# Optimization experiments

Hardware: AMD Instinct MI355X
Metric: run time of the kernel (lower is better)

Reference implementation:

```python
import jax, jax.numpy as jnp
import numpy as np
import math

NSEG = 4
SAMPLE_RATE = 16  # curve samples per bezier segment
SHARPNESS = 150.0


def _control_radians():
    n = NSEG
    theta = math.pi * 2 / (4 * n) + math.atan(math.tan(2 * math.pi / (4 * n)) / 3)
    r = []
    for i in range(n):
        r += [2 * math.pi / n * i, 2 * math.pi / n * i + theta, 2 * math.pi / n * (i + 1) - theta]
    return jnp.asarray(np.asarray(r, dtype=np.float32).reshape(n, 3))


def sdf_extruded_bezier(quaternion, translation, points, control_polygon, bez_weights, height):
    # quaternion [B,K,4], translation [B,K,3], points [B,M,3],
    # control_polygon [B,K,nseg,3,2], bez_weights [B,K,nseg,2], height [B,K]
    B, K, _ = quaternion.shape
    p = points[:, :, None, :] - translation[:, None, :, :]            # [B,M,K,3]
    q = quaternion[:, None, :, :]
    qn = q / jnp.sqrt(jnp.sum(q * q, -1, keepdims=True) + 1e-8)
    w, qv = qn[..., :1], -qn[..., 1:]                                  # conjugate -> world->local
    t2 = 2.0 * jnp.cross(qv, p)
    pl = p + w * t2 + jnp.cross(qv, t2)                                # local coords [B,M,K,3]
    p2d, pz = pl[..., :2], pl[..., 2]
    # rational cubic bezier per segment: P0,P1,P2 from this segment, P3 = next segment's P0
    P0 = control_polygon[:, :, :, 0, :]
    P1 = control_polygon[:, :, :, 1, :]
    P2 = control_polygon[:, :, :, 2, :]
    P3 = jnp.roll(P0, -1, axis=2)
    ts = jnp.linspace(0.0, 1.0, SAMPLE_RATE, endpoint=False)           # [S]
    b0 = (1 - ts) ** 3
    b1 = 3 * (1 - ts) ** 2 * ts
    b2 = 3 * (1 - ts) * ts ** 2
    b3 = ts ** 3
    w1 = bez_weights[..., 0:1]                                          # [B,K,nseg,1]
    w2 = bez_weights[..., 1:2]
    den = b0 + w1 * b1 + w2 * b2 + b3                                   # [B,K,nseg,S]
    num = (P0[..., None, :] * b0[:, None]
           + P1[..., None, :] * (w1[..., None] * b1[:, None])
           + P2[..., None, :] * (w2[..., None] * b2[:, None])
           + P3[..., None, :] * b3[:, None])                            # [B,K,nseg,S,2]
    curve = (num / den[..., None]).reshape(B, K, NSEG * SAMPLE_RATE, 2)
    rel = curve[:, None] - p2d[..., None, :]                            # [B,M,K,S*nseg,2]
    d2 = jnp.sum(rel * rel, -1)
    dmin = jnp.sqrt(jnp.min(d2, -1) + 1e-12)                            # unsigned 2D distance
    nxt = jnp.roll(rel, -1, axis=-2)
    cross = rel[..., 0] * nxt[..., 1] - rel[..., 1] * nxt[..., 0]
    dot = jnp.sum(rel * nxt, -1)
    winding = jnp.sum(jnp.arctan2(cross, dot), -1) / (2 * math.pi)
    sdf2d = jnp.where(jnp.abs(winding) > 0.5, -dmin, dmin)
    dz = jnp.abs(pz) - jnp.abs(height)[:, None, :]
    sdf = (jnp.minimum(jnp.maximum(sdf2d, dz), 0.0)
           + jnp.sqrt(jnp.maximum(sdf2d, 0.0) ** 2 + jnp.maximum(dz, 0.0) ** 2 + 1e-12))
    return sdf, dmin


def setup_inputs() -> dict:
    key = jax.random.key(0)
    k1, k2, k3, k4 = jax.random.split(key, 4)
    B, M, K, C = 4, 2048, 64, 64
    P = 4 + 3 + 1 + NSEG * 3 + NSEG * 2  # 28
    return {
        "sample_point_coordinates": jax.random.uniform(k1, (B, M, 3), jnp.float32, -1.0, 1.0),
        "primitive_parameters": 0.3 * jax.random.normal(k2, (B, P, K), jnp.float32),
        "intersection_layer_weights": jax.random.uniform(k3, (B, K, C), jnp.float32),
        "union_layer_weights": jax.random.uniform(k4, (B, C), jnp.float32),
        "is_training": 1,
    }


def reference(sample_point_coordinates, primitive_parameters, intersection_layer_weights, union_layer_weights, is_training):
    pp = jnp.swapaxes(primitive_parameters, 1, 2)                       # [B,K,P]
    B, K, _ = pp.shape
    quaternion = pp[..., :4]
    translation = pp[..., 4:7]
    height = pp[..., 7]
    radius = jnp.abs(pp[..., 8:8 + NSEG * 3]).reshape(B, K, NSEG, 3)
    rad = _control_radians()[None, None]                                # [1,1,nseg,3]
    control_polygon = jnp.stack([jnp.cos(rad) * radius, jnp.sin(rad) * radius], -1)
    bez_weights = jnp.abs(pp[..., 8 + NSEG * 3:]).reshape(B, K, NSEG, 2)
    primitive_sdf, support_distances = sdf_extruded_bezier(
        quaternion, translation, sample_point_coordinates, control_polygon, bez_weights, height)
    primitive_occ = jax.nn.sigmoid(-primitive_sdf * SHARPNESS)          # [B,M,K]
    # occupancy_pre_intersection = w*occ + (1-w)*1 = 1 - w*(1-occ), fused
    w_int = intersection_layer_weights[:, None]                         # [B,1,K,C]
    pre_i = 1.0 - w_int * (1.0 - primitive_occ[..., None])              # [B,M,K,C]
    if is_training:
        sw = jax.lax.stop_gradient(jax.nn.softmax(pre_i * -40.0, axis=-2))
        inter = jnp.sum(sw * pre_i, -2)                                 # soft-min -> [B,M,C]
    else:
        inter = jnp.min(pre_i, -2)
    pre_u = union_layer_weights[:, None, :] * inter
    if is_training:
        sw2 = jax.lax.stop_gradient(jax.nn.softmax(pre_u * 40.0, axis=-1))
        occupancies = jnp.sum(sw2 * pre_u, -1)                          # soft-max -> [B,M]
    else:
        occupancies = jnp.max(pre_u, -1)
    return occupancies, primitive_sdf, inter, support_distances
```

## Files before the change

kernel.cpp:

```cpp
#include <hip/hip_runtime.h>
#include <math.h>


#define NB 4
#define NM 2048
#define NK 64
#define NC 64
#define NS 64
#define PPB 4

#define OCC_OFF   0
#define SDF_OFF   8192
#define INTER_OFF 532480
#define SUP_OFF   1056768

#define CT 0.86285621096f
#define ST 0.50544946275f

#define L2E_40  57.70780163555852f
#define L2E_150 216.40425613334447f

__global__ __launch_bounds__(256) void curve_table_kernel(
    const float* __restrict__ pp,
    float2* __restrict__ wcurve)
{
    const int b    = blockIdx.x;
    const int lane = threadIdx.x & 63;
    const int seg  = threadIdx.x >> 6;
    const int nseg = (seg + 1) & 3;
    const float* __restrict__ ppb = pp + b * (28 * NK);
    const int k = lane;

    const float r0 = fabsf(ppb[(8 + seg * 3 + 0) * NK + k]);
    const float r1 = fabsf(ppb[(8 + seg * 3 + 1) * NK + k]);
    const float r2 = fabsf(ppb[(8 + seg * 3 + 2) * NK + k]);
    const float rn = fabsf(ppb[(8 + nseg * 3 + 0) * NK + k]);
    const float w1 = fabsf(ppb[(20 + seg * 2 + 0) * NK + k]);
    const float w2 = fabsf(ppb[(20 + seg * 2 + 1) * NK + k]);

    const float c0x[4] = { 1.f, 0.f, -1.f,  0.f };
    const float c0y[4] = { 0.f, 1.f,  0.f, -1.f };
    const float c1x[4] = {  CT, -ST, -CT,  ST };
    const float c1y[4] = {  ST,  CT, -ST, -CT };
    const float c2x[4] = {  ST, -CT, -ST,  CT };
    const float c2y[4] = {  CT,  ST, -CT, -ST };

    const float P0x = c0x[seg] * r0,  P0y = c0y[seg] * r0;
    const float P1x = c1x[seg] * r1,  P1y = c1y[seg] * r1;
    const float P2x = c2x[seg] * r2,  P2y = c2y[seg] * r2;
    const float P3x = c0x[nseg] * rn, P3y = c0y[nseg] * rn;

    #pragma unroll
    for (int j = 0; j < 16; ++j) {
        const float t  = (float)j * 0.0625f;
        const float u  = 1.f - t;
        const float b0 = u * u * u;
        const float b1 = 3.f * u * u * t;
        const float b2 = 3.f * u * t * t;
        const float b3 = t * t * t;
        const float wb1 = w1 * b1, wb2 = w2 * b2;
        const float inv = __builtin_amdgcn_rcpf(b0 + wb1 + wb2 + b3);
        const int s = seg * 16 + j;
        wcurve[(b * NS + s) * NK + k] = make_float2(
            (P0x * b0 + P1x * wb1 + P2x * wb2 + P3x * b3) * inv,
            (P0y * b0 + P1y * wb1 + P2y * wb2 + P3y * b3) * inv);
    }
}

__global__ __launch_bounds__(256) void extrude_net_kernel(
    const float* __restrict__ pts,
    const float* __restrict__ pp,
    const float* __restrict__ Wint,
    const float* __restrict__ Uw,
    const float2* __restrict__ wcurve,
    float* __restrict__ out)
{
    __shared__ __align__(16) float2 s_curve[NS][NK];
    __shared__ float s_om[PPB][NK];

    const int tid  = threadIdx.x;
    const int lane = tid & 63;
    const int wv   = tid >> 6;
    const int gpt  = blockIdx.x * PPB + wv;
    const int b    = gpt >> 11;
    const float* __restrict__ ppb = pp + b * (28 * NK);

    {
        const float4* __restrict__ src = (const float4*)wcurve + b * (NS * NK / 2);
        float4* dst = (float4*)&s_curve[0][0];
        #pragma unroll
        for (int i = 0; i < 8; ++i)
            dst[i * 256 + tid] = src[i * 256 + tid];
    }
    __syncthreads();

    const float ptx = pts[gpt * 3 + 0];
    const float pty = pts[gpt * 3 + 1];
    const float ptz = pts[gpt * 3 + 2];
    {
        const int k = lane;
        const float q0 = ppb[0 * NK + k], q1 = ppb[1 * NK + k];
        const float q2 = ppb[2 * NK + k], q3 = ppb[3 * NK + k];
        const float trx = ppb[4 * NK + k], try_ = ppb[5 * NK + k], trz = ppb[6 * NK + k];
        const float h   = ppb[7 * NK + k];

        const float px = ptx - trx, py = pty - try_, pz = ptz - trz;
        const float inv = __builtin_amdgcn_rsqf(q0 * q0 + q1 * q1 + q2 * q2 + q3 * q3 + 1e-8f);
        const float w  = q0 * inv;
        const float vx = -q1 * inv, vy = -q2 * inv, vz = -q3 * inv;
        const float t2x = 2.f * (vy * pz - vz * py);
        const float t2y = 2.f * (vz * px - vx * pz);
        const float t2z = 2.f * (vx * py - vy * px);
        const float plx = px + w * t2x + (vy * t2z - vz * t2y);
        const float ply = py + w * t2y + (vz * t2x - vx * t2z);
        const float plz = pz + w * t2z + (vx * t2y - vy * t2x);

        const float2* __restrict__ col = &s_curve[0][k];

        const float2 cfirst = col[0];
        float rx = cfirst.x - plx;
        float ry = cfirst.y - ply;
        const float r0x = rx, r0y = ry;
        bool apos = ry > 0.f;
        const bool pos0 = apos;
        int   wn  = 0;
        float d2a = rx * rx + ry * ry;
        float d2b = 3.4e38f;
        #pragma unroll
        for (int s = 1; s < NS; ++s) {
            const float2 cn = col[s * NK];
            const float nx = cn.x - plx;
            const float ny = cn.y - ply;
            const float cr = rx * ny - ry * nx;
            const bool bpos = ny > 0.f;
            const bool cpos = cr > 0.f;
            const bool cneg = cr < 0.f;
            wn += ((!apos) & bpos & cpos) ? 1 : 0;
            wn -= (apos & (!bpos) & cneg) ? 1 : 0;
            const float d2 = nx * nx + ny * ny;
            if (s & 1) d2b = fminf(d2b, d2); else d2a = fminf(d2a, d2);
            apos = bpos; rx = nx; ry = ny;
        }
        {
            const float cr = rx * r0y - ry * r0x;
            wn += ((!apos) & pos0 & (cr > 0.f)) ? 1 : 0;
            wn -= (apos & (!pos0) & (cr < 0.f)) ? 1 : 0;
        }
        const float dmin  = sqrtf(fminf(d2a, d2b) + 1e-12f);
        const float sdf2d = (wn != 0) ? -dmin : dmin;
        const float dz    = fabsf(plz) - fabsf(h);
        const float mx    = fmaxf(sdf2d, dz);
        const float e1    = fmaxf(sdf2d, 0.f);
        const float e2    = fmaxf(dz, 0.f);
        const float sdf   = fminf(mx, 0.f) + sqrtf(e1 * e1 + e2 * e2 + 1e-12f);

        out[SDF_OFF + gpt * NK + k] = sdf;
        out[SUP_OFF + gpt * NK + k] = dmin;
        s_om[wv][k] = __builtin_amdgcn_rcpf(1.f + exp2f(-sdf * L2E_150));
    }
    __syncthreads();

    {
        const float4* __restrict__ wsrc = (const float4*)(Wint + b * (NK * NC));
        float4* wdst = (float4*)&s_curve[0][0];
        #pragma unroll
        for (int i = 0; i < 4; ++i)
            wdst[i * 256 + tid] = wsrc[i * 256 + tid];
    }
    __syncthreads();

    {
        const int c = lane;
        const float* __restrict__ WbL = (const float*)&s_curve[0][0];
        const float* __restrict__ omw = s_om[wv];
        float srun = 0.f, trun = 0.f;
        #pragma unroll
        for (int kk = 0; kk < NK; ++kk) {
            const float om  = omw[kk];
            const float pre = fmaf(-WbL[kk * NC + c], om, 1.f);
            const float e   = exp2f(pre * -L2E_40);
            srun += e;
            trun = fmaf(e, pre, trun);
        }
        const float inter = trun * __builtin_amdgcn_rcpf(srun);
        out[INTER_OFF + gpt * NC + c] = inter;

        const float pu = Uw[b * NC + c] * inter;
        float umax = pu;
        #pragma unroll
        for (int off = 32; off > 0; off >>= 1)
            umax = fmaxf(umax, __shfl_xor(umax, off, 64));
        const float e = exp2f((pu - umax) * L2E_40);
        float s1 = e, s2 = e * pu;
        #pragma unroll
        for (int off = 32; off > 0; off >>= 1) {
            s1 += __shfl_xor(s1, off, 64);
            s2 += __shfl_xor(s2, off, 64);
        }
        if (lane == 0) out[OCC_OFF + gpt] = s2 * __builtin_amdgcn_rcpf(s1);
    }
}

extern "C" void kernel_launch(void* const* d_in, const int* in_sizes, int n_in,
                              void* d_out, int out_size, void* d_ws, size_t ws_size,
                              hipStream_t stream) {
    const float* pts  = (const float*)d_in[0];
    const float* pp   = (const float*)d_in[1];
    const float* Wint = (const float*)d_in[2];
    const float* Uw   = (const float*)d_in[3];
    float*  out    = (float*)d_out;
    float2* wcurve = (float2*)d_ws;

    curve_table_kernel<<<NB, 256, 0, stream>>>(pp, wcurve);
    const int grid = (NB * NM) / PPB;
    extrude_net_kernel<<<grid, 256, 0, stream>>>(pts, pp, Wint, Uw, wcurve, out);
}
```

Baseline: 89.81 us.

## Fuse curve table into main kernel with float4 sample pairs and shuffles

Removes the separate curve-table kernel. Each block now recomputes the rational Bezier samples per batch directly into shared memory, which drops a launch and the global round trip, at the cost of redundant curve math in every block. Samples are stored as float4 pairs so the winding/distance loop reads two samples per LDS access. Per-primitive occupancy is broadcast with wave shuffles instead of a shared array.

After: 88.78 us. No clear change (-1.1%).

```diff
diff --git a/kernel.cpp b/kernel.cpp
--- a/kernel.cpp
+++ b/kernel.cpp
@@ -20,63 +20,14 @@
 #define L2E_40  57.70780163555852f
 #define L2E_150 216.40425613334447f
 
-__global__ __launch_bounds__(256) void curve_table_kernel(
-    const float* __restrict__ pp,
-    float2* __restrict__ wcurve)
-{
-    const int b    = blockIdx.x;
-    const int lane = threadIdx.x & 63;
-    const int seg  = threadIdx.x >> 6;
-    const int nseg = (seg + 1) & 3;
-    const float* __restrict__ ppb = pp + b * (28 * NK);
-    const int k = lane;
-
-    const float r0 = fabsf(ppb[(8 + seg * 3 + 0) * NK + k]);
-    const float r1 = fabsf(ppb[(8 + seg * 3 + 1) * NK + k]);
-    const float r2 = fabsf(ppb[(8 + seg * 3 + 2) * NK + k]);
-    const float rn = fabsf(ppb[(8 + nseg * 3 + 0) * NK + k]);
-    const float w1 = fabsf(ppb[(20 + seg * 2 + 0) * NK + k]);
-    const float w2 = fabsf(ppb[(20 + seg * 2 + 1) * NK + k]);
-
-    const float c0x[4] = { 1.f, 0.f, -1.f,  0.f };
-    const float c0y[4] = { 0.f, 1.f,  0.f, -1.f };
-    const float c1x[4] = {  CT, -ST, -CT,  ST };
-    const float c1y[4] = {  ST,  CT, -ST, -CT };
-    const float c2x[4] = {  ST, -CT, -ST,  CT };
-    const float c2y[4] = {  CT,  ST, -CT, -ST };
-
-    const float P0x = c0x[seg] * r0,  P0y = c0y[seg] * r0;
-    const float P1x = c1x[seg] * r1,  P1y = c1y[seg] * r1;
-    const float P2x = c2x[seg] * r2,  P2y = c2y[seg] * r2;
-    const float P3x = c0x[nseg] * rn, P3y = c0y[nseg] * rn;
-
-    #pragma unroll
-    for (int j = 0; j < 16; ++j) {
-        const float t  = (float)j * 0.0625f;
-        const float u  = 1.f - t;
-        const float b0 = u * u * u;
-        const float b1 = 3.f * u * u * t;
-        const float b2 = 3.f * u * t * t;
-        const float b3 = t * t * t;
-        const float wb1 = w1 * b1, wb2 = w2 * b2;
-        const float inv = __builtin_amdgcn_rcpf(b0 + wb1 + wb2 + b3);
-        const int s = seg * 16 + j;
-        wcurve[(b * NS + s) * NK + k] = make_float2(
-            (P0x * b0 + P1x * wb1 + P2x * wb2 + P3x * b3) * inv,
-            (P0y * b0 + P1y * wb1 + P2y * wb2 + P3y * b3) * inv);
-    }
-}
-
-__global__ __launch_bounds__(256) void extrude_net_kernel(
+__global__ __launch_bounds__(256) void extrude_net_fused(
     const float* __restrict__ pts,
     const float* __restrict__ pp,
     const float* __restrict__ Wint,
     const float* __restrict__ Uw,
-    const float2* __restrict__ wcurve,
     float* __restrict__ out)
 {
-    __shared__ __align__(16) float2 s_curve[NS][NK];
-    __shared__ float s_om[PPB][NK];
+    __shared__ __align__(16) float4 s_curve4[NS / 2][NK];
 
     const int tid  = threadIdx.x;
     const int lane = tid & 63;
@@ -84,21 +35,50 @@
     const int gpt  = blockIdx.x * PPB + wv;
     const int b    = gpt >> 11;
     const float* __restrict__ ppb = pp + b * (28 * NK);
-
-    {
-        const float4* __restrict__ src = (const float4*)wcurve + b * (NS * NK / 2);
-        float4* dst = (float4*)&s_curve[0][0];
-        #pragma unroll
-        for (int i = 0; i < 8; ++i)
-            dst[i * 256 + tid] = src[i * 256 + tid];
+    const int k = lane;
+
+    {
+        const int seg = wv;
+        const float r0 = fabsf(ppb[(8 + seg * 3 + 0) * NK + k]);
+        const float r1 = fabsf(ppb[(8 + seg * 3 + 1) * NK + k]);
+        const float r2 = fabsf(ppb[(8 + seg * 3 + 2) * NK + k]);
+        const float rn = fabsf(ppb[(8 + ((seg + 1) & 3) * 3 + 0) * NK + k]);
+        const float w1 = fabsf(ppb[(20 + seg * 2 + 0) * NK + k]);
+        const float w2 = fabsf(ppb[(20 + seg * 2 + 1) * NK + k]);
+
+        const float cosv = (seg == 0) ? 1.f : (seg == 2) ? -1.f : 0.f;
+        const float sinv = (seg == 1) ? 1.f : (seg == 3) ? -1.f : 0.f;
+        const float P0x =  r0 * cosv,            P0y = r0 * sinv;
+        const float P1x = (CT * cosv - ST * sinv) * r1, P1y = (CT * sinv + ST * cosv) * r1;
+        const float P2x = (ST * cosv - CT * sinv) * r2, P2y = (ST * sinv + CT * cosv) * r2;
+        const float P3x = -rn * sinv,            P3y = rn * cosv;
+
+        #pragma unroll
+        for (int j = 0; j < 16; j += 2) {
+            float sx[2], sy[2];
+            #pragma unroll
+            for (int h = 0; h < 2; ++h) {
+                const float t  = (float)(j + h) * 0.0625f;
+                const float u  = 1.f - t;
+                const float b0 = u * u * u;
+                const float b1 = 3.f * u * u * t;
+                const float b2 = 3.f * u * t * t;
+                const float b3 = t * t * t;
+                const float wb1 = w1 * b1, wb2 = w2 * b2;
+                const float inv = __builtin_amdgcn_rcpf(b0 + wb1 + wb2 + b3);
+                sx[h] = (P0x * b0 + P1x * wb1 + P2x * wb2 + P3x * b3) * inv;
+                sy[h] = (P0y * b0 + P1y * wb1 + P2y * wb2 + P3y * b3) * inv;
+            }
+            s_curve4[seg * 8 + (j >> 1)][k] = make_float4(sx[0], sy[0], sx[1], sy[1]);
+        }
     }
     __syncthreads();
 
     const float ptx = pts[gpt * 3 + 0];
     const float pty = pts[gpt * 3 + 1];
     const float ptz = pts[gpt * 3 + 2];
-    {
-        const int k = lane;
+    float om;
+    {
         const float q0 = ppb[0 * NK + k], q1 = ppb[1 * NK + k];
         const float q2 = ppb[2 * NK + k], q3 = ppb[3 * NK + k];
         const float trx = ppb[4 * NK + k], try_ = ppb[5 * NK + k], trz = ppb[6 * NK + k];
@@ -115,34 +95,40 @@
         const float ply = py + w * t2y + (vz * t2x - vx * t2z);
         const float plz = pz + w * t2z + (vx * t2y - vy * t2x);
 
-        const float2* __restrict__ col = &s_curve[0][k];
-
-        const float2 cfirst = col[0];
-        float rx = cfirst.x - plx;
-        float ry = cfirst.y - ply;
-        const float r0x = rx, r0y = ry;
+        const float4* __restrict__ col = &s_curve4[0][k];
+
+        const float4 c0 = col[0];
+        const float ax = c0.x - plx, ay = c0.y - ply;
+        float rx = c0.z - plx, ry = c0.w - ply;
+        const bool pos0 = ay > 0.f;
         bool apos = ry > 0.f;
-        const bool pos0 = apos;
-        int   wn  = 0;
-        float d2a = rx * rx + ry * ry;
-        float d2b = 3.4e38f;
-        #pragma unroll
-        for (int s = 1; s < NS; ++s) {
-            const float2 cn = col[s * NK];
-            const float nx = cn.x - plx;
-            const float ny = cn.y - ply;
-            const float cr = rx * ny - ry * nx;
-            const bool bpos = ny > 0.f;
-            const bool cpos = cr > 0.f;
-            const bool cneg = cr < 0.f;
-            wn += ((!apos) & bpos & cpos) ? 1 : 0;
-            wn -= (apos & (!bpos) & cneg) ? 1 : 0;
-            const float d2 = nx * nx + ny * ny;
-            if (s & 1) d2b = fminf(d2b, d2); else d2a = fminf(d2a, d2);
-            apos = bpos; rx = nx; ry = ny;
-        }
+        int wn = 0;
         {
-            const float cr = rx * r0y - ry * r0x;
+            const float cr = ax * ry - ay * rx;
+            wn += ((!pos0) & apos & (cr > 0.f)) ? 1 : 0;
+            wn -= (pos0 & (!apos) & (cr < 0.f)) ? 1 : 0;
+        }
+        float d2a = ax * ax + ay * ay;
+        float d2b = rx * rx + ry * ry;
+        #pragma unroll
+        for (int s2 = 1; s2 < 32; ++s2) {
+            const float4 cn = col[s2 * NK];
+            const float nx0 = cn.x - plx, ny0 = cn.y - ply;
+            const float nx1 = cn.z - plx, ny1 = cn.w - ply;
+            const bool b0p = ny0 > 0.f;
+            const bool b1p = ny1 > 0.f;
+            const float cr0 = rx * ny0 - ry * nx0;
+            const float cr1 = nx0 * ny1 - ny0 * nx1;
+            wn += ((!apos) & b0p & (cr0 > 0.f)) ? 1 : 0;
+            wn -= (apos & (!b0p) & (cr0 < 0.f)) ? 1 : 0;
+            wn += ((!b0p) & b1p & (cr1 > 0.f)) ? 1 : 0;
+            wn -= (b0p & (!b1p) & (cr1 < 0.f)) ? 1 : 0;
+            d2a = fminf(d2a, nx0 * nx0 + ny0 * ny0);
+            d2b = fminf(d2b, nx1 * nx1 + ny1 * ny1);
+            apos = b1p; rx = nx1; ry = ny1;
+        }
+        {
+            const float cr = rx * ay - ry * ax;
             wn += ((!apos) & pos0 & (cr > 0.f)) ? 1 : 0;
             wn -= (apos & (!pos0) & (cr < 0.f)) ? 1 : 0;
         }
@@ -156,13 +142,13 @@
 
         out[SDF_OFF + gpt * NK + k] = sdf;
         out[SUP_OFF + gpt * NK + k] = dmin;
-        s_om[wv][k] = __builtin_amdgcn_rcpf(1.f + exp2f(-sdf * L2E_150));
+        om = __builtin_amdgcn_rcpf(1.f + exp2f(-sdf * L2E_150));
     }
     __syncthreads();
 
     {
         const float4* __restrict__ wsrc = (const float4*)(Wint + b * (NK * NC));
-        float4* wdst = (float4*)&s_curve[0][0];
+        float4* wdst = (float4*)&s_curve4[0][0];
         #pragma unroll
         for (int i = 0; i < 4; ++i)
             wdst[i * 256 + tid] = wsrc[i * 256 + tid];
@@ -171,13 +157,12 @@
 
     {
         const int c = lane;
-        const float* __restrict__ WbL = (const float*)&s_curve[0][0];
-        const float* __restrict__ omw = s_om[wv];
+        const float* __restrict__ WbL = (const float*)&s_curve4[0][0];
         float srun = 0.f, trun = 0.f;
         #pragma unroll
         for (int kk = 0; kk < NK; ++kk) {
-            const float om  = omw[kk];
-            const float pre = fmaf(-WbL[kk * NC + c], om, 1.f);
+            const float omk = __shfl(om, kk, 64);
+            const float pre = fmaf(-WbL[kk * NC + c], omk, 1.f);
             const float e   = exp2f(pre * -L2E_40);
             srun += e;
             trun = fmaf(e, pre, trun);
@@ -208,10 +193,9 @@
     const float* pp   = (const float*)d_in[1];
     const float* Wint = (const float*)d_in[2];
     const float* Uw   = (const float*)d_in[3];
-    float*  out    = (float*)d_out;
-    float2* wcurve = (float2*)d_ws;
-
-    curve_table_kernel<<<NB, 256, 0, stream>>>(pp, wcurve);
+    float* out = (float*)d_out;
+    (void)d_ws; (void)ws_size;
+
     const int grid = (NB * NM) / PPB;
-    extrude_net_kernel<<<grid, 256, 0, stream>>>(pts, pp, Wint, Uw, wcurve, out);
+    extrude_net_fused<<<grid, 256, 0, stream>>>(pts, pp, Wint, Uw, out);
 }
```
